# Kernel optimization log

Measured on AMD Instinct MI355X. Metric: run time of the kernel, lower is better.

The kernel has to match this reference:

```python
import math
import jax, jax.numpy as jnp
import numpy as np

H = 2048
T = 8192
NUM_LAYERS = 24
LAYER_ID = 6


def setup_inputs() -> dict:
    key = jax.random.key(0)
    ks = jax.random.split(key, 5)
    ratio_0_to_1 = LAYER_ID / (NUM_LAYERS - 1)
    ratio_1_to_almost_0 = 1.0 - LAYER_ID / NUM_LAYERS
    # parameter init exactly as in RwkvSelfAttention.__init__
    zigzag = 0.5 * (jnp.arange(1, H + 1) % 3 - 1)
    time_first = jnp.full((H,), math.log(0.3), jnp.float32) + zigzag.astype(jnp.float32)
    hh = jnp.arange(0, H, dtype=jnp.float32)
    time_decay = -5.0 + 8.0 * (hh / (H - 1)) ** (0.7 + 1.3 * ratio_0_to_1)
    xx = jnp.arange(H, dtype=jnp.float32) / H
    time_mix_key = jnp.power(xx, ratio_1_to_almost_0)
    time_mix_value = time_mix_key + 0.3 * ratio_0_to_1
    time_mix_receptance = jnp.power(xx, 0.5 * ratio_1_to_almost_0)
    scale = 1.0 / math.sqrt(H)
    return {
        "hidden": jax.random.normal(ks[0], (T, H), jnp.float32),
        "sx": jnp.zeros((H,), jnp.float32),
        "aa": jnp.zeros((H,), jnp.float32),
        "bb": jnp.zeros((H,), jnp.float32),
        "pp": jnp.full((H,), -1e30, jnp.float32),  # log-space -inf init
        "time_decay": time_decay,
        "time_first": time_first,
        "time_mix_key": time_mix_key,
        "time_mix_value": time_mix_value,
        "time_mix_receptance": time_mix_receptance,
        "Wk": jax.random.normal(ks[1], (H, H), jnp.float32) * scale,
        "Wv": jax.random.normal(ks[2], (H, H), jnp.float32) * scale,
        "Wr": jax.random.normal(ks[3], (H, H), jnp.float32) * scale,
        "Wo": jax.random.normal(ks[4], (H, H), jnp.float32) * scale,
    }


def reference(hidden, sx, aa, bb, pp, time_decay, time_first, time_mix_key,
              time_mix_value, time_mix_receptance, Wk, Wv, Wr, Wo):
    # token-shift mix: c_x[t] = hidden[t-1], c_x[0] = sx
    c_x = jnp.concatenate((sx[None, :], hidden[:-1, :]), axis=0)  # [T, H]
    key_x = hidden * time_mix_key + c_x * (1.0 - time_mix_key)
    value_x = hidden * time_mix_value + c_x * (1.0 - time_mix_value)
    receptance_x = hidden * time_mix_receptance + c_x * (1.0 - time_mix_receptance)

    r = jax.nn.sigmoid(receptance_x @ Wr)  # [T, H]
    k = key_x @ Wk                         # [T, H]
    v = value_x @ Wv                       # [T, H]

    w_decay = -jnp.exp(time_decay)  # [H]

    def step(state, kv):
        a, b, p = state
        kk, vv = kv
        # output with bonus (time_first)
        ww = time_first + kk
        q = jnp.maximum(p, ww)
        e1 = jnp.exp(p - q)
        e2 = jnp.exp(ww - q)
        out_t = (e1 * a + e2 * vv) / (e1 * b + e2)
        # state update with decay
        ww2 = w_decay + p
        q2 = jnp.maximum(ww2, kk)
        e1b = jnp.exp(ww2 - q2)
        e2b = jnp.exp(kk - q2)
        return (e1b * a + e2b * vv, e1b * b + e2b, q2), out_t

    (aa, bb, pp), wkv = jax.lax.scan(step, (aa, bb, pp), (k, v))  # wkv: [T, H]

    out = hidden + (r * wkv) @ Wo
    return out, hidden[-1, :], aa, bb, pp
```

## Files before the change

kernel.cpp:

```cpp
#include <hip/hip_runtime.h>
#include <stdint.h>

#define H 2048
#define T 8192
#define C_CH 128
#define L_CH 64

typedef unsigned short u16;
typedef unsigned int u32;

__device__ __forceinline__ float bf2f(u16 u) {
  return __uint_as_float(((u32)u) << 16);
}
__device__ __forceinline__ u16 f2bf(float f) {
  u32 u = __float_as_uint(f);
  u = u + 0x7FFFu + ((u >> 16) & 1u);
  return (u16)(u >> 16);
}
__device__ __forceinline__ bool in_is_bf16(const u32* ppw) {
  u32 w = ppw[0];
  return (w >> 16) == (w & 0xFFFFu);
}
__device__ __forceinline__ float ldin(const void* p, size_t i, bool bf) {
  return bf ? bf2f(((const u16*)p)[i]) : ((const float*)p)[i];
}
__device__ __forceinline__ void stout(void* p, size_t i, float v, bool bf) {
  if (bf) ((u16*)p)[i] = f2bf(v);
  else ((float*)p)[i] = v;
}

__global__ void mix3_kernel(const void* __restrict__ hidden,
                            const void* __restrict__ sx,
                            const void* __restrict__ tmk,
                            const void* __restrict__ tmv,
                            const void* __restrict__ tmr,
                            u16* __restrict__ outk, u16* __restrict__ outv,
                            u16* __restrict__ outr, const u32* __restrict__ ppw) {
  bool bf = in_is_bf16(ppw);
  int i = blockIdx.x * blockDim.x + threadIdx.x;
  int h = i & (H - 1);
  float hv = ldin(hidden, (size_t)i, bf);
  float cv = (i < H) ? ldin(sx, (size_t)h, bf) : ldin(hidden, (size_t)i - H, bf);
  float d = hv - cv;
  outk[i] = f2bf(cv + ldin(tmk, (size_t)h, bf) * d);
  outv[i] = f2bf(cv + ldin(tmv, (size_t)h, bf) * d);
  outr[i] = f2bf(cv + ldin(tmr, (size_t)h, bf) * d);
}

__global__ void transpose_kernel(const void* __restrict__ W, u16* __restrict__ Wt,
                                 const u32* __restrict__ ppw) {
  bool bf = in_is_bf16(ppw);
  __shared__ u16 tile[32][33];
  int bx = blockIdx.x * 32, by = blockIdx.y * 32;
  int tx = threadIdx.x, ty = threadIdx.y;
#pragma unroll
  for (int j = 0; j < 32; j += 8)
    tile[ty + j][tx] = f2bf(ldin(W, (size_t)(by + ty + j) * H + bx + tx, bf));
  __syncthreads();
#pragma unroll
  for (int j = 0; j < 32; j += 8)
    Wt[(size_t)(bx + ty + j) * H + by + tx] = tile[tx][ty + j];
}

typedef short bf16x8 __attribute__((ext_vector_type(8)));
typedef float f32x4 __attribute__((ext_vector_type(4)));

#define MODE_K 0
#define MODE_BF16 1
#define MODE_SIG 2
#define MODE_ADDH 3

__device__ __forceinline__ void gl_lds16(const short* g, short* l) {
  __builtin_amdgcn_global_load_lds((__attribute__((address_space(1))) void*)(g),
                                   (__attribute__((address_space(3))) void*)(l),
                                   16, 0, 0);
}

__device__ __forceinline__ void stage_ht(const short* g, size_t koff,
                                         short* slot, int wid) {
  gl_lds16(g + koff, slot + wid * 1024);
  gl_lds16(g + koff + (size_t)16 * H, slot + wid * 1024 + 512);
}

template <int MODE>
__global__ __launch_bounds__(512, 2) void gemm_kernel(
    const u16* __restrict__ Au, const u16* __restrict__ Btu,
    void* __restrict__ C, const void* __restrict__ hid,
    const u32* __restrict__ ppw) {
  __shared__ alignas(16) short As[4][256 * 32];
  __shared__ alignas(16) short Bs[4][256 * 32];
  const short* A = (const short*)Au;
  const short* Bt = (const short*)Btu;

  const int bid = blockIdx.x;
  const int xcd = bid & 7;
  const int s = bid >> 3;
  const int mblk = (xcd << 2) | (s & 3);
  const int nblk = s >> 2;
  const int m0 = mblk * 256;
  const int n0 = nblk * 256;

  const int tid = threadIdx.x;
  const int lane = tid & 63;
  const int wid = tid >> 6;
  const int wm = wid >> 2;
  const int wn = wid & 3;
  const int lrow = lane & 15;
  const int quad = lane >> 4;

  const int srow = lane >> 2;
  const int scol = (lane & 3) * 8;
  const short* gA = A + (size_t)(m0 + wid * 32 + srow) * H + scol;
  const short* gB = Bt + (size_t)(n0 + wid * 32 + srow) * H + scol;

  const int aoff = (wm * 128 + lrow) * 32 + quad * 8;
  const int boff = (wn * 64 + lrow) * 32 + quad * 8;

  f32x4 acc[8][4];
#pragma unroll
  for (int i = 0; i < 8; i++)
#pragma unroll
    for (int j = 0; j < 4; j++) acc[i][j] = (f32x4){0.f, 0.f, 0.f, 0.f};

  const int NT = H / 64;

  stage_ht(gA, 0, As[0], wid);
  stage_ht(gB, 0, Bs[0], wid);
  stage_ht(gA, 32, As[1], wid);
  stage_ht(gB, 32, Bs[1], wid);
  stage_ht(gA, 64, As[2], wid);
  stage_ht(gB, 64, Bs[2], wid);
  stage_ht(gA, 96, As[3], wid);
  stage_ht(gB, 96, Bs[3], wid);
  asm volatile("s_waitcnt vmcnt(8)" ::: "memory");
  __builtin_amdgcn_sched_barrier(0);
  __builtin_amdgcn_s_barrier();

  bf16x8 af[4], bfg[4];

#define PHASE_CORE(ks, mh, BREAD, STAGE_STMT, DRAIN_STMT)                     \
  {                                                                           \
    const short* aslot = &As[(b << 1) | (ks)][0];                             \
    _Pragma("unroll") for (int ii = 0; ii < 4; ii++)                          \
        af[ii] = *(const bf16x8*)(aslot + aoff + (mh)*2048 + ii * 512);       \
    if (BREAD) {                                                              \
      const short* bslot = &Bs[(b << 1) | (ks)][0];                           \
      _Pragma("unroll") for (int j = 0; j < 4; j++)                           \
          bfg[j] = *(const bf16x8*)(bslot + boff + j * 512);                  \
    }                                                                         \
    STAGE_STMT;                                                               \
    __builtin_amdgcn_s_barrier();                                             \
    asm volatile("s_waitcnt lgkmcnt(0)" ::: "memory");                        \
    __builtin_amdgcn_sched_barrier(0);                                        \
    __builtin_amdgcn_s_setprio(1);                                            \
    _Pragma("unroll") for (int ii = 0; ii < 4; ii++)                          \
      _Pragma("unroll") for (int j = 0; j < 4; j++)                           \
          acc[(mh)*4 + ii][j] = __builtin_amdgcn_mfma_f32_16x16x32_bf16(      \
              af[ii], bfg[j], acc[(mh)*4 + ii][j], 0, 0, 0);                  \
    __builtin_amdgcn_s_setprio(0);                                            \
    DRAIN_STMT;                                                               \
    __builtin_amdgcn_s_barrier();                                             \
  }

  for (int tau = 0; tau < NT; ++tau) {
    const int b = tau & 1;
    const int bo = b ^ 1;

    PHASE_CORE(0, 0, true,
               { if (tau >= 1 && tau <= NT - 2)
                   stage_ht(gA, (size_t)(tau + 1) * 64 + 32, &As[(bo << 1) | 1][0], wid); },
               {})
    PHASE_CORE(0, 1, false,
               { if (tau >= 1 && tau <= NT - 2)
                   stage_ht(gB, (size_t)(tau + 1) * 64 + 32, &Bs[(bo << 1) | 1][0], wid); },
               {
                 if (tau == NT - 1) { asm volatile("s_waitcnt vmcnt(0)" ::: "memory"); }
                 else               { asm volatile("s_waitcnt vmcnt(8)" ::: "memory"); }
                 __builtin_amdgcn_sched_barrier(0);
               })
    PHASE_CORE(1, 0, true,
               { if (tau <= NT - 3)
                   stage_ht(gA, (size_t)(tau + 2) * 64, &As[(b << 1) | 0][0], wid); },
               {})
    PHASE_CORE(1, 1, false,
               { if (tau <= NT - 3)
                   stage_ht(gB, (size_t)(tau + 2) * 64, &Bs[(b << 1) | 0][0], wid); },
               {
                 if (tau == NT - 2) { asm volatile("s_waitcnt vmcnt(4)" ::: "memory"); }
                 else               { asm volatile("s_waitcnt vmcnt(8)" ::: "memory"); }
                 __builtin_amdgcn_sched_barrier(0);
               })
  }
#undef PHASE_CORE

  bool bf = (MODE == MODE_ADDH) ? in_is_bf16(ppw) : true;
#pragma unroll
  for (int i = 0; i < 8; i++) {
#pragma unroll
    for (int j = 0; j < 4; j++) {
#pragma unroll
      for (int reg = 0; reg < 4; reg++) {
        int row = m0 + wm * 128 + i * 16 + quad * 4 + reg;
        int col = n0 + wn * 64 + j * 16 + lrow;
        size_t idx = (size_t)row * H + col;
        float val = acc[i][j][reg];
        if (MODE == MODE_K || MODE == MODE_BF16) {
          ((u16*)C)[idx] = f2bf(val);
        } else if (MODE == MODE_SIG) {
          ((u16*)C)[idx] = f2bf(1.0f / (1.0f + __expf(-val)));
        } else {
          stout(C, idx, val + ldin(hid, idx, bf), bf);
        }
      }
    }
  }
}

__global__ __launch_bounds__(256) void wkv_local_kernel(
    const u16* __restrict__ kbuf, const u16* __restrict__ vbuf,
    const void* __restrict__ tdec,
    float* __restrict__ suma, float* __restrict__ sumb, float* __restrict__ sump,
    const u32* __restrict__ ppw) {
  bool bf = in_is_bf16(ppw);
  int h = blockIdx.x * 256 + threadIdx.x;
  int c = blockIdx.y;
  float w = -__expf(ldin(tdec, h, bf));
  float a = 0.f, b = 0.f, p = -1e30f;
  size_t base = (size_t)c * L_CH * H + h;
#pragma unroll 4
  for (int t = 0; t < L_CH; t++) {
    size_t idx = base + (size_t)t * H;
    float kk = bf2f(kbuf[idx]);
    float vv = bf2f(vbuf[idx]);
    float ww2 = w + p;
    float q2 = fmaxf(ww2, kk);
    float e1b = __expf(ww2 - q2), e2b = __expf(kk - q2);
    a = e1b * a + e2b * vv;
    b = e1b * b + e2b;
    p = q2;
  }
  suma[(size_t)c * H + h] = a;
  sumb[(size_t)c * H + h] = b;
  sump[(size_t)c * H + h] = p;
}

__global__ __launch_bounds__(256) void wkv_prefix_kernel(
    const float* __restrict__ suma, const float* __restrict__ sumb,
    const float* __restrict__ sump,
    const void* __restrict__ aa_in, const void* __restrict__ bb_in,
    const void* __restrict__ pp_in, const void* __restrict__ tdec,
    const void* __restrict__ hidden,
    float* __restrict__ sta, float* __restrict__ stb, float* __restrict__ stp,
    void* __restrict__ dout, const u32* __restrict__ ppw) {
  bool bf = in_is_bf16(ppw);
  int h = blockIdx.x * 256 + threadIdx.x;
  float a = ldin(aa_in, h, bf), b = ldin(bb_in, h, bf), p = ldin(pp_in, h, bf);
  float w = -__expf(ldin(tdec, h, bf));
  float wL = w * (float)L_CH;
  for (int c = 0; c < C_CH; c++) {
    size_t i = (size_t)c * H + h;
    sta[i] = a;
    stb[i] = b;
    stp[i] = p;
    float la = suma[i], lb = sumb[i], lp = sump[i];
    float pd = p + wL;
    float q = fmaxf(pd, lp);
    float e1 = __expf(pd - q), e2 = __expf(lp - q);
    a = e1 * a + e2 * la;
    b = e1 * b + e2 * lb;
    p = q;
  }
  size_t base = (size_t)T * H;
  stout(dout, base + h, ldin(hidden, (size_t)(T - 1) * H + h, bf), bf);
  stout(dout, base + H + h, a, bf);
  stout(dout, base + 2 * H + h, b, bf);
  stout(dout, base + 3 * H + h, p, bf);
}

__global__ __launch_bounds__(256) void wkv_out_kernel(
    const u16* __restrict__ kbuf, const u16* __restrict__ vbuf,
    const u16* __restrict__ rbuf,
    const float* __restrict__ sta, const float* __restrict__ stb,
    const float* __restrict__ stp,
    const void* __restrict__ tdec, const void* __restrict__ tfirst,
    u16* __restrict__ rw, const u32* __restrict__ ppw) {
  bool bf = in_is_bf16(ppw);
  int h = blockIdx.x * 256 + threadIdx.x;
  int c = blockIdx.y;
  size_t si = (size_t)c * H + h;
  float a = sta[si], b = stb[si], p = stp[si];
  float tf = ldin(tfirst, h, bf);
  float w = -__expf(ldin(tdec, h, bf));
  size_t base = (size_t)c * L_CH * H + h;
#pragma unroll 4
  for (int t = 0; t < L_CH; t++) {
    size_t idx = base + (size_t)t * H;
    float kk = bf2f(kbuf[idx]);
    float vv = bf2f(vbuf[idx]);
    float rr = bf2f(rbuf[idx]);
    float ww = tf + kk;
    float q = fmaxf(p, ww);
    float e1 = __expf(p - q), e2 = __expf(ww - q);
    float wkv = (e1 * a + e2 * vv) / (e1 * b + e2);
    rw[idx] = f2bf(rr * wkv);
    float ww2 = w + p;
    float q2 = fmaxf(ww2, kk);
    float e1b = __expf(ww2 - q2), e2b = __expf(kk - q2);
    a = e1b * a + e2b * vv;
    b = e1b * b + e2b;
    p = q2;
  }
}

extern "C" void kernel_launch(void* const* d_in, const int* in_sizes, int n_in,
                              void* d_out, int out_size, void* d_ws, size_t ws_size,
                              hipStream_t stream) {
  const void* hidden = d_in[0];
  const void* sx = d_in[1];
  const void* aa = d_in[2];
  const void* bb = d_in[3];
  const void* pp = d_in[4];
  const void* tdec = d_in[5];
  const void* tfirst = d_in[6];
  const void* tmk = d_in[7];
  const void* tmv = d_in[8];
  const void* tmr = d_in[9];
  const void* Wk = d_in[10];
  const void* Wv = d_in[11];
  const void* Wr = d_in[12];
  const void* Wo = d_in[13];
  const u32* ppw = (const u32*)d_in[4];

  char* ws = (char*)d_ws;
  const size_t TH2 = (size_t)T * H * 2;
  const size_t WT2 = (size_t)H * H * 2;
  u16* A1 = (u16*)ws;
  u16* A2 = (u16*)(ws + TH2);
  u16* A3 = (u16*)(ws + 2 * TH2);
  u16* B1 = (u16*)(ws + 3 * TH2);
  u16* Wt_buf = (u16*)(ws + 4 * TH2);
  float* suma = (float*)(ws + 4 * TH2 + WT2);
  float* sumb = suma + (size_t)C_CH * H;
  float* sump = sumb + (size_t)C_CH * H;
  float* sta = sump + (size_t)C_CH * H;
  float* stb = sta + (size_t)C_CH * H;
  float* stp = stb + (size_t)C_CH * H;

  dim3 mixG((T * H) / 256), mixB(256);
  dim3 trG(64, 64), trB(32, 8);
  dim3 gG(256), gB(512);
  dim3 scG(H / 256, C_CH), scB(256);

  mix3_kernel<<<mixG, mixB, 0, stream>>>(hidden, sx, tmk, tmv, tmr,
                                         A1, A2, A3, ppw);
  transpose_kernel<<<trG, trB, 0, stream>>>(Wr, Wt_buf, ppw);
  gemm_kernel<MODE_SIG><<<gG, gB, 0, stream>>>(A3, Wt_buf, B1, nullptr, ppw);
  transpose_kernel<<<trG, trB, 0, stream>>>(Wk, Wt_buf, ppw);
  gemm_kernel<MODE_K><<<gG, gB, 0, stream>>>(A1, Wt_buf, A3, nullptr, ppw);
  transpose_kernel<<<trG, trB, 0, stream>>>(Wv, Wt_buf, ppw);
  gemm_kernel<MODE_BF16><<<gG, gB, 0, stream>>>(A2, Wt_buf, A1, nullptr, ppw);
  wkv_local_kernel<<<scG, scB, 0, stream>>>(A3, A1, tdec, suma, sumb, sump, ppw);
  wkv_prefix_kernel<<<dim3(H / 256), scB, 0, stream>>>(
      suma, sumb, sump, aa, bb, pp, tdec, hidden, sta, stb, stp, d_out, ppw);
  wkv_out_kernel<<<scG, scB, 0, stream>>>(A3, A1, B1, sta, stb, stp,
                                          tdec, tfirst, A2, ppw);
  transpose_kernel<<<trG, trB, 0, stream>>>(Wo, Wt_buf, ppw);
  gemm_kernel<MODE_ADDH><<<gG, gB, 0, stream>>>(A2, Wt_buf, d_out, hidden, ppw);
}
```

Measured before the change: 656.5 us.

## Swizzle LDS tiles, restructure GEMM phases, stage epilogue through LDS for coalesced stores

Applies an XOR swizzle to the LDS layout of A/B tiles (both on global-to-LDS staging and fragment reads) to reduce bank conflicts. Restructures the main loop so A fragments for both M-halves and B are loaded together per k-slice, halving the barrier count per k-step. Rewrites the epilogue to transpose accumulators through LDS so each lane writes two contiguous elements, giving coalesced global stores and vectorized residual loads. Risks include extra register pressure from holding more fragments and reuse of the As buffer for the epilogue while other waves may still read it.

```diff
diff --git a/kernel.cpp b/kernel.cpp
--- a/kernel.cpp
+++ b/kernel.cpp
@@ -64,6 +64,7 @@
 
 typedef short bf16x8 __attribute__((ext_vector_type(8)));
 typedef float f32x4 __attribute__((ext_vector_type(4)));
+typedef float f32x2 __attribute__((ext_vector_type(2)));
 
 #define MODE_K 0
 #define MODE_BF16 1
@@ -109,12 +110,13 @@
   const int quad = lane >> 4;
 
   const int srow = lane >> 2;
-  const int scol = (lane & 3) * 8;
-  const short* gA = A + (size_t)(m0 + wid * 32 + srow) * H + scol;
-  const short* gB = Bt + (size_t)(n0 + wid * 32 + srow) * H + scol;
-
-  const int aoff = (wm * 128 + lrow) * 32 + quad * 8;
-  const int boff = (wn * 64 + lrow) * 32 + quad * 8;
+  const int schunk = (lane & 3) ^ ((lane >> 3) & 3);
+  const short* gA = A + (size_t)(m0 + wid * 32 + srow) * H + schunk * 8;
+  const short* gB = Bt + (size_t)(n0 + wid * 32 + srow) * H + schunk * 8;
+
+  const int gxor = (quad ^ ((lrow >> 1) & 3)) * 8;
+  const int arow = (wm * 128 + lrow) * 32 + gxor;
+  const int brow = (wn * 64 + lrow) * 32 + gxor;
 
   f32x4 acc[8][4];
 #pragma unroll
@@ -136,80 +138,133 @@
   __builtin_amdgcn_sched_barrier(0);
   __builtin_amdgcn_s_barrier();
 
-  bf16x8 af[4], bfg[4];
-
-#define PHASE_CORE(ks, mh, BREAD, STAGE_STMT, DRAIN_STMT)                     \
-  {                                                                           \
-    const short* aslot = &As[(b << 1) | (ks)][0];                             \
-    _Pragma("unroll") for (int ii = 0; ii < 4; ii++)                          \
-        af[ii] = *(const bf16x8*)(aslot + aoff + (mh)*2048 + ii * 512);       \
-    if (BREAD) {                                                              \
-      const short* bslot = &Bs[(b << 1) | (ks)][0];                           \
-      _Pragma("unroll") for (int j = 0; j < 4; j++)                           \
-          bfg[j] = *(const bf16x8*)(bslot + boff + j * 512);                  \
-    }                                                                         \
-    STAGE_STMT;                                                               \
-    __builtin_amdgcn_s_barrier();                                             \
-    asm volatile("s_waitcnt lgkmcnt(0)" ::: "memory");                        \
-    __builtin_amdgcn_sched_barrier(0);                                        \
-    __builtin_amdgcn_s_setprio(1);                                            \
-    _Pragma("unroll") for (int ii = 0; ii < 4; ii++)                          \
-      _Pragma("unroll") for (int j = 0; j < 4; j++)                           \
-          acc[(mh)*4 + ii][j] = __builtin_amdgcn_mfma_f32_16x16x32_bf16(      \
-              af[ii], bfg[j], acc[(mh)*4 + ii][j], 0, 0, 0);                  \
-    __builtin_amdgcn_s_setprio(0);                                            \
-    DRAIN_STMT;                                                               \
-    __builtin_amdgcn_s_barrier();                                             \
-  }
-
   for (int tau = 0; tau < NT; ++tau) {
     const int b = tau & 1;
     const int bo = b ^ 1;
-
-    PHASE_CORE(0, 0, true,
-               { if (tau >= 1 && tau <= NT - 2)
-                   stage_ht(gA, (size_t)(tau + 1) * 64 + 32, &As[(bo << 1) | 1][0], wid); },
-               {})
-    PHASE_CORE(0, 1, false,
-               { if (tau >= 1 && tau <= NT - 2)
-                   stage_ht(gB, (size_t)(tau + 1) * 64 + 32, &Bs[(bo << 1) | 1][0], wid); },
-               {
-                 if (tau == NT - 1) { asm volatile("s_waitcnt vmcnt(0)" ::: "memory"); }
-                 else               { asm volatile("s_waitcnt vmcnt(8)" ::: "memory"); }
-                 __builtin_amdgcn_sched_barrier(0);
-               })
-    PHASE_CORE(1, 0, true,
-               { if (tau <= NT - 3)
-                   stage_ht(gA, (size_t)(tau + 2) * 64, &As[(b << 1) | 0][0], wid); },
-               {})
-    PHASE_CORE(1, 1, false,
-               { if (tau <= NT - 3)
-                   stage_ht(gB, (size_t)(tau + 2) * 64, &Bs[(b << 1) | 0][0], wid); },
-               {
-                 if (tau == NT - 2) { asm volatile("s_waitcnt vmcnt(4)" ::: "memory"); }
-                 else               { asm volatile("s_waitcnt vmcnt(8)" ::: "memory"); }
-                 __builtin_amdgcn_sched_barrier(0);
-               })
+    const short* a0s = &As[(b << 1) | 0][0];
+    const short* b0s = &Bs[(b << 1) | 0][0];
+    const short* a1s = &As[(b << 1) | 1][0];
+    const short* b1s = &Bs[(b << 1) | 1][0];
+
+    bf16x8 af0[4], af1[4], bfr[4];
+
+#pragma unroll
+    for (int i = 0; i < 4; i++)
+      af0[i] = *(const bf16x8*)(a0s + arow + i * 512);
+#pragma unroll
+    for (int j = 0; j < 4; j++)
+      bfr[j] = *(const bf16x8*)(b0s + brow + j * 512);
+#pragma unroll
+    for (int i = 0; i < 4; i++)
+      af1[i] = *(const bf16x8*)(a0s + arow + 2048 + i * 512);
+    if (tau >= 1 && tau <= NT - 2)
+      stage_ht(gA, (size_t)(tau + 1) * 64 + 32, &As[(bo << 1) | 1][0], wid);
+    __builtin_amdgcn_s_setprio(1);
+#pragma unroll
+    for (int i = 0; i < 4; i++)
+#pragma unroll
+      for (int j = 0; j < 4; j++)
+        acc[i][j] = __builtin_amdgcn_mfma_f32_16x16x32_bf16(af0[i], bfr[j],
+                                                            acc[i][j], 0, 0, 0);
+    __builtin_amdgcn_s_setprio(0);
+    __builtin_amdgcn_s_barrier();
+
+    if (tau >= 1 && tau <= NT - 2)
+      stage_ht(gB, (size_t)(tau + 1) * 64 + 32, &Bs[(bo << 1) | 1][0], wid);
+    __builtin_amdgcn_s_setprio(1);
+#pragma unroll
+    for (int i = 0; i < 4; i++)
+#pragma unroll
+      for (int j = 0; j < 4; j++)
+        acc[4 + i][j] = __builtin_amdgcn_mfma_f32_16x16x32_bf16(
+            af1[i], bfr[j], acc[4 + i][j], 0, 0, 0);
+    __builtin_amdgcn_s_setprio(0);
+    if (tau == NT - 1) { asm volatile("s_waitcnt vmcnt(0)" ::: "memory"); }
+    else               { asm volatile("s_waitcnt vmcnt(8)" ::: "memory"); }
+    __builtin_amdgcn_sched_barrier(0);
+    __builtin_amdgcn_s_barrier();
+
+#pragma unroll
+    for (int i = 0; i < 4; i++)
+      af0[i] = *(const bf16x8*)(a1s + arow + i * 512);
+#pragma unroll
+    for (int j = 0; j < 4; j++)
+      bfr[j] = *(const bf16x8*)(b1s + brow + j * 512);
+#pragma unroll
+    for (int i = 0; i < 4; i++)
+      af1[i] = *(const bf16x8*)(a1s + arow + 2048 + i * 512);
+    if (tau <= NT - 3)
+      stage_ht(gA, (size_t)(tau + 2) * 64, &As[(b << 1) | 0][0], wid);
+    __builtin_amdgcn_s_setprio(1);
+#pragma unroll
+    for (int i = 0; i < 4; i++)
+#pragma unroll
+      for (int j = 0; j < 4; j++)
+        acc[i][j] = __builtin_amdgcn_mfma_f32_16x16x32_bf16(af0[i], bfr[j],
+                                                            acc[i][j], 0, 0, 0);
+    __builtin_amdgcn_s_setprio(0);
+    __builtin_amdgcn_s_barrier();
+
+    if (tau <= NT - 3)
+      stage_ht(gB, (size_t)(tau + 2) * 64, &Bs[(b << 1) | 0][0], wid);
+    __builtin_amdgcn_s_setprio(1);
+#pragma unroll
+    for (int i = 0; i < 4; i++)
+#pragma unroll
+      for (int j = 0; j < 4; j++)
+        acc[4 + i][j] = __builtin_amdgcn_mfma_f32_16x16x32_bf16(
+            af1[i], bfr[j], acc[4 + i][j], 0, 0, 0);
+    __builtin_amdgcn_s_setprio(0);
+    if (tau == NT - 2) { asm volatile("s_waitcnt vmcnt(4)" ::: "memory"); }
+    else               { asm volatile("s_waitcnt vmcnt(8)" ::: "memory"); }
+    __builtin_amdgcn_sched_barrier(0);
+    __builtin_amdgcn_s_barrier();
   }
-#undef PHASE_CORE
-
-  bool bf = (MODE == MODE_ADDH) ? in_is_bf16(ppw) : true;
-#pragma unroll
-  for (int i = 0; i < 8; i++) {
-#pragma unroll
-    for (int j = 0; j < 4; j++) {
-#pragma unroll
-      for (int reg = 0; reg < 4; reg++) {
-        int row = m0 + wm * 128 + i * 16 + quad * 4 + reg;
-        int col = n0 + wn * 64 + j * 16 + lrow;
+
+  {
+    bool bf = (MODE == MODE_ADDH) ? in_is_bf16(ppw) : true;
+    float* lC = (float*)&As[0][0] + (size_t)wid * (32 * 66);
+    const int el = lane & 31;
+    const int eh = lane >> 5;
+#pragma unroll
+    for (int p = 0; p < 4; p++) {
+#pragma unroll
+      for (int ih = 0; ih < 2; ih++) {
+        const int i = p * 2 + ih;
+#pragma unroll
+        for (int j = 0; j < 4; j++)
+#pragma unroll
+          for (int reg = 0; reg < 4; reg++)
+            lC[(ih * 16 + quad * 4 + reg) * 66 + j * 16 + lrow] =
+                acc[i][j][reg];
+      }
+#pragma unroll
+      for (int k = 0; k < 16; k++) {
+        const int rr = k * 2 + eh;
+        f32x2 v = *(const f32x2*)(lC + rr * 66 + el * 2);
+        const int row = m0 + wm * 128 + p * 32 + rr;
+        const int col = n0 + wn * 64 + el * 2;
         size_t idx = (size_t)row * H + col;
-        float val = acc[i][j][reg];
-        if (MODE == MODE_K || MODE == MODE_BF16) {
-          ((u16*)C)[idx] = f2bf(val);
-        } else if (MODE == MODE_SIG) {
-          ((u16*)C)[idx] = f2bf(1.0f / (1.0f + __expf(-val)));
+        if (MODE == MODE_SIG) {
+          v[0] = 1.0f / (1.0f + __expf(-v[0]));
+          v[1] = 1.0f / (1.0f + __expf(-v[1]));
+        }
+        if (MODE == MODE_ADDH) {
+          if (bf) {
+            u32 hv = *(const u32*)((const u16*)hid + idx);
+            v[0] += bf2f((u16)(hv & 0xFFFFu));
+            v[1] += bf2f((u16)(hv >> 16));
+            u32 pk = (u32)f2bf(v[0]) | ((u32)f2bf(v[1]) << 16);
+            *(u32*)((u16*)C + idx) = pk;
+          } else {
+            f32x2 hv = *(const f32x2*)((const float*)hid + idx);
+            v[0] += hv[0];
+            v[1] += hv[1];
+            *(f32x2*)((float*)C + idx) = v;
+          }
         } else {
-          stout(C, idx, val + ldin(hid, idx, bf), bf);
+          u32 pk = (u32)f2bf(v[0]) | ((u32)f2bf(v[1]) << 16);
+          *(u32*)((u16*)C + idx) = pk;
         }
       }
     }
```

Result: faster. 617.5 us (-5.9%).
